# Kernel optimization log

Measured on AMD Instinct MI355X. Metric: run time of the kernel, lower is better.

Reference implementation:

```python
import jax, jax.numpy as jnp
import numpy as np

# Module config: RoDAlignMax(aligned_height=9, aligned_width=9, spatial_scale=0.25)
# Internally RoDAlignFunction is called with aligned_height+1, aligned_width+1,
# then max_pool2d(kernel=2, stride=1) shrinks each spatial dim by 1.
AH, AW = 10, 10          # pre-pool sampling grid (aligned_{h,w} + 1)
SPATIAL_SCALE = 0.25


def _rod_align(features, rois, ah, aw, scale):
    """RoDAlign: uniform bilinear sampling grid over the WHOLE feature map,
    with samples falling INSIDE the ROI zeroed out (region-of-discard).
    features: [B,C,H,W], rois: [R,5]=(batch_ind,x1,y1,x2,y2) -> [R,C,ah,aw]."""
    B, C, H, W = features.shape
    dt = features.dtype
    bidx = rois[:, 0].astype(jnp.int32)                              # [R]
    x1 = rois[:, 1] * scale
    y1 = rois[:, 2] * scale
    x2 = rois[:, 3] * scale
    y2 = rois[:, 4] * scale
    # uniform grid spanning the full feature map
    h = jnp.arange(ah, dtype=dt) * ((H - 1.0) / (ah - 1.0))          # [AH]
    w = jnp.arange(aw, dtype=dt) * ((W - 1.0) / (aw - 1.0))          # [AW]
    h0 = jnp.minimum(jnp.floor(h), H - 2).astype(jnp.int32)
    w0 = jnp.minimum(jnp.floor(w), W - 2).astype(jnp.int32)
    hr = (h - h0.astype(dt))[:, None, None]                          # [AH,1,1]
    wr = (w - w0.astype(dt))[None, :, None]                          # [1,AW,1]
    b = bidx[:, None, None]                                          # [R,1,1]
    hi0 = h0[None, :, None]; hi1 = hi0 + 1                           # [1,AH,1]
    wi0 = w0[None, None, :]; wi1 = wi0 + 1                           # [1,1,AW]
    # four corner gathers; advanced idx dims go first -> [R,AH,AW,C]
    ul = features[b, :, hi0, wi0]
    ur = features[b, :, hi0, wi1]
    dl = features[b, :, hi1, wi0]
    dr = features[b, :, hi1, wi1]
    out = (ul * (1 - hr) * (1 - wr) + ur * (1 - hr) * wr
           + dl * hr * (1 - wr) + dr * hr * wr)                      # [R,AH,AW,C]
    # zero samples inside the ROI (the kept crop region is discarded)
    in_h = (h[None, :] >= y1[:, None]) & (h[None, :] <= y2[:, None])  # [R,AH]
    in_w = (w[None, :] >= x1[:, None]) & (w[None, :] <= x2[:, None])  # [R,AW]
    inside = in_h[:, :, None] & in_w[:, None, :]                      # [R,AH,AW]
    out = jnp.where(inside[..., None], jnp.zeros((), dt), out)
    return jnp.transpose(out, (0, 3, 1, 2))                           # [R,C,AH,AW]


def _maxpool2x2_s1(x):
    # max_pool2d(kernel_size=2, stride=1) on [..., H, W]
    return jnp.maximum(jnp.maximum(x[..., :-1, :-1], x[..., :-1, 1:]),
                       jnp.maximum(x[..., 1:, :-1], x[..., 1:, 1:]))


def setup_inputs() -> dict:
    key = jax.random.key(0)
    k1, k2, k3, k4, k5 = jax.random.split(key, 5)
    B, C, H, W = 4, 256, 64, 64
    R = 2048
    img = H / SPATIAL_SCALE  # 256.0, input-image coordinate extent
    features = jax.random.normal(k1, (B, C, H, W), dtype=jnp.float32)
    bidx = jax.random.randint(k2, (R,), 0, B).astype(jnp.float32)
    x1 = jax.random.uniform(k3, (R,), dtype=jnp.float32) * (img * 0.5)
    y1 = jax.random.uniform(k4, (R,), dtype=jnp.float32) * (img * 0.5)
    wh = jax.random.uniform(k5, (R, 2), dtype=jnp.float32) * (img * 0.45) + img * 0.05
    x2 = jnp.minimum(x1 + wh[:, 0], img - 1.0)
    y2 = jnp.minimum(y1 + wh[:, 1], img - 1.0)
    rois = jnp.stack([bidx, x1, y1, x2, y2], axis=1)  # [R,5]
    return {"features": features, "rois": rois}


def reference(features, rois):
    x = _rod_align(features, rois, AH, AW, SPATIAL_SCALE)  # [R,C,10,10]
    return _maxpool2x2_s1(x)                               # [R,C,9,9]
```

## Files before the change

### kernel.cpp

```cpp
#include <hip/hip_runtime.h>


#define NB 4
#define NC 256
#define HW 64
#define NR 2048

__global__ __launch_bounds__(256) void rod_gather(const float* __restrict__ F,
                                                  float* __restrict__ G) {
    int idx = blockIdx.x * 256 + threadIdx.x;
    int c = idx & 255;
    int t = idx >> 8;
    int p = t % 100;
    int b = t / 100;
    int i = p / 10, j = p - i * 10;
    G[idx] = F[((b * NC + c) << 12) + i * 448 + j * 7];
}

__global__ __launch_bounds__(128) void rod_main(const float* __restrict__ G,
                                                const float* __restrict__ rois,
                                                float* __restrict__ out) {
    __shared__ float lds[128 * 83];
    const int tid  = threadIdx.x;
    const int r    = blockIdx.x >> 1;
    const int half = blockIdx.x & 1;
    const int c    = half * 128 + tid;

    const float x1 = rois[r * 5 + 1] * 0.25f;
    const float y1 = rois[r * 5 + 2] * 0.25f;
    const float x2 = rois[r * 5 + 3] * 0.25f;
    const float y2 = rois[r * 5 + 4] * 0.25f;
    const int  b   = (int)rois[r * 5 + 0];

    bool inw[10], inh[10];
    #pragma unroll
    for (int j = 0; j < 10; ++j) {
        float s = 7.0f * (float)j;
        inw[j] = (s >= x1) && (s <= x2);
        inh[j] = (s >= y1) && (s <= y2);
    }

    const float* gb = G + (size_t)b * 100 * NC + c;

    float vprev[10];
    #pragma unroll
    for (int j = 0; j < 10; ++j) {
        float g = gb[j * NC];
        vprev[j] = (inh[0] && inw[j]) ? 0.0f : g;
    }
    #pragma unroll
    for (int i = 1; i < 10; ++i) {
        float vcur[10];
        #pragma unroll
        for (int j = 0; j < 10; ++j) {
            float g = gb[(i * 10 + j) * NC];
            vcur[j] = (inh[i] && inw[j]) ? 0.0f : g;
        }
        float rm[10];
        #pragma unroll
        for (int j = 0; j < 10; ++j) rm[j] = fmaxf(vprev[j], vcur[j]);
        #pragma unroll
        for (int j = 0; j < 9; ++j)
            lds[tid * 83 + (i - 1) * 9 + j] = fmaxf(rm[j], rm[j + 1]);
        #pragma unroll
        for (int j = 0; j < 10; ++j) vprev[j] = vcur[j];
    }
    __syncthreads();

    float* dst = out + (size_t)r * 20736 + half * 10368;
    #pragma unroll 9
    for (int k = 0; k < 81; ++k) {
        int el = tid + (k << 7);
        int cc = (int)((unsigned)el / 81u);
        dst[el] = lds[el + cc * 2];
    }
}

extern "C" void kernel_launch(void* const* d_in, const int* in_sizes, int n_in,
                              void* d_out, int out_size, void* d_ws, size_t ws_size,
                              hipStream_t stream) {
    const float* F    = (const float*)d_in[0];
    const float* rois = (const float*)d_in[1];
    float*       out  = (float*)d_out;
    float*       G    = (float*)d_ws;

    rod_gather<<<dim3(400), dim3(256), 0, stream>>>(F, G);
    rod_main<<<dim3(NR * 2), dim3(128), 0, stream>>>(G, rois, out);
}
```

Baseline: 184.6 us.

## Use 64-thread blocks, float4 output stores, and prefetch next gather row

Each ROI is now split into four 64-channel blocks instead of two 128-channel ones. The LDS tile is unpadded (stride 81), so the staging buffer can be copied to global memory with contiguous float4 stores instead of scalar stores that needed a per-element divide. Global loads for the next row of samples are issued one iteration ahead to hide latency. The trade-off is that the unpadded stride-81 LDS writes may see more bank conflicts, and the per-thread prefetch buffer raises register use.

```diff
diff --git a/kernel.cpp b/kernel.cpp
--- a/kernel.cpp
+++ b/kernel.cpp
@@ -17,14 +17,14 @@
     G[idx] = F[((b * NC + c) << 12) + i * 448 + j * 7];
 }
 
-__global__ __launch_bounds__(128) void rod_main(const float* __restrict__ G,
-                                                const float* __restrict__ rois,
-                                                float* __restrict__ out) {
-    __shared__ float lds[128 * 83];
-    const int tid  = threadIdx.x;
-    const int r    = blockIdx.x >> 1;
-    const int half = blockIdx.x & 1;
-    const int c    = half * 128 + tid;
+__global__ __launch_bounds__(64) void rod_main(const float* __restrict__ G,
+                                               const float* __restrict__ rois,
+                                               float* __restrict__ out) {
+    __shared__ __align__(16) float lds[64 * 81];
+    const int tid = threadIdx.x;
+    const int r   = blockIdx.x >> 2;
+    const int q   = blockIdx.x & 3;
+    const int c   = (q << 6) + tid;
 
     const float x1 = rois[r * 5 + 1] * 0.25f;
     const float y1 = rois[r * 5 + 2] * 0.25f;
@@ -42,38 +42,50 @@
 
     const float* gb = G + (size_t)b * 100 * NC + c;
 
+    float raw1[10];
     float vprev[10];
-    #pragma unroll
-    for (int j = 0; j < 10; ++j) {
-        float g = gb[j * NC];
-        vprev[j] = (inh[0] && inw[j]) ? 0.0f : g;
+    {
+        float raw0[10];
+        #pragma unroll
+        for (int j = 0; j < 10; ++j) raw0[j] = gb[j * NC];
+        #pragma unroll
+        for (int j = 0; j < 10; ++j) raw1[j] = gb[(10 + j) * NC];
+        #pragma unroll
+        for (int j = 0; j < 10; ++j) vprev[j] = (inh[0] && inw[j]) ? 0.0f : raw0[j];
     }
+
     #pragma unroll
     for (int i = 1; i < 10; ++i) {
+        float rawn[10];
+        if (i < 9) {
+            #pragma unroll
+            for (int j = 0; j < 10; ++j) rawn[j] = gb[((i + 1) * 10 + j) * NC];
+        }
         float vcur[10];
         #pragma unroll
-        for (int j = 0; j < 10; ++j) {
-            float g = gb[(i * 10 + j) * NC];
-            vcur[j] = (inh[i] && inw[j]) ? 0.0f : g;
-        }
+        for (int j = 0; j < 10; ++j) vcur[j] = (inh[i] && inw[j]) ? 0.0f : raw1[j];
         float rm[10];
         #pragma unroll
         for (int j = 0; j < 10; ++j) rm[j] = fmaxf(vprev[j], vcur[j]);
         #pragma unroll
         for (int j = 0; j < 9; ++j)
-            lds[tid * 83 + (i - 1) * 9 + j] = fmaxf(rm[j], rm[j + 1]);
+            lds[tid * 81 + (i - 1) * 9 + j] = fmaxf(rm[j], rm[j + 1]);
         #pragma unroll
         for (int j = 0; j < 10; ++j) vprev[j] = vcur[j];
+        if (i < 9) {
+            #pragma unroll
+            for (int j = 0; j < 10; ++j) raw1[j] = rawn[j];
+        }
     }
     __syncthreads();
 
-    float* dst = out + (size_t)r * 20736 + half * 10368;
-    #pragma unroll 9
-    for (int k = 0; k < 81; ++k) {
-        int el = tid + (k << 7);
-        int cc = (int)((unsigned)el / 81u);
-        dst[el] = lds[el + cc * 2];
-    }
+    const float4* lds4 = reinterpret_cast<const float4*>(lds);
+    float4* dst4 = reinterpret_cast<float4*>(out + (size_t)r * 20736 + q * 5184);
+    #pragma unroll
+    for (int k = 0; k < 20; ++k)
+        dst4[tid + (k << 6)] = lds4[tid + (k << 6)];
+    if (tid < 16)
+        dst4[tid + 1280] = lds4[tid + 1280];
 }
 
 extern "C" void kernel_launch(void* const* d_in, const int* in_sizes, int n_in,
@@ -85,5 +97,5 @@
     float*       G    = (float*)d_ws;
 
     rod_gather<<<dim3(400), dim3(256), 0, stream>>>(F, G);
-    rod_main<<<dim3(NR * 2), dim3(128), 0, stream>>>(G, rois, out);
+    rod_main<<<dim3(NR * 4), dim3(64), 0, stream>>>(G, rois, out);
 }
```

Result: faster. 178.3 us (-3.4%).
